# Kernel optimization log

Measured on AMD Instinct MI355X. Metric: run time of the kernel, lower is better.

The kernel has to match this reference:

```python
import jax, jax.numpy as jnp
import numpy as np

B, L, E, H = 2, 2048, 1024, 16
D = E // H  # 64


def setup_inputs() -> dict:
    key = jax.random.key(0)
    ks = jax.random.split(key, 9)
    return {
        "query": jax.random.normal(ks[0], (B, L, E), dtype=jnp.float32),
        "value": jax.random.normal(ks[1], (B, L, E), dtype=jnp.float32),
        "key": jax.random.normal(ks[2], (B, L, E), dtype=jnp.float32),
        "mask": jax.random.randint(ks[3], (B, 1, L, L), 0, 2, dtype=jnp.int32),
        "Wq": jax.random.normal(ks[4], (D, D), dtype=jnp.float32) * 0.05,
        "Wk": jax.random.normal(ks[5], (D, D), dtype=jnp.float32) * 0.05,
        "Wv": jax.random.normal(ks[6], (D, D), dtype=jnp.float32) * 0.05,
        "Wfc": jax.random.normal(ks[7], (E, E), dtype=jnp.float32) * 0.02,
        "bfc": jax.random.normal(ks[8], (E,), dtype=jnp.float32) * 0.02,
    }


def reference(query, value, key, mask, Wq, Wk, Wv, Wfc, bfc):
    b, q_len, _ = query.shape
    k_len = key.shape[1]
    v_len = value.shape[1]
    # split heads: [b, l, H, D]
    q = query.reshape(b, q_len, H, D)
    k = key.reshape(b, k_len, H, D)
    v = value.reshape(b, v_len, H, D)
    # per-head linear projections (shared weights across heads, no bias)
    q = jnp.einsum('bqhd,ed->bqhe', q, Wq)
    k = jnp.einsum('bkhd,ed->bkhe', k, Wk)
    v = jnp.einsum('bvhd,ed->bvhe', v, Wv)
    # attention scores [b, H, q, k]
    attn = jnp.einsum('bqhd,bkhd->bhqk', q, k)
    # NOTE: original masks BEFORE scaling, and scales by sqrt(embedding_size)
    attn = jnp.where(mask == 0, jnp.float32(-1e20), attn)
    attn = attn / jnp.float32(E ** 0.5)
    attn = jax.nn.softmax(attn, axis=3)
    out = jnp.einsum('bhqk,bkhd->bqhd', attn, v).reshape(b, q_len, E)
    out = out @ Wfc.T + bfc
    return out
```

## Files before the change

### kernel.cpp

```cpp
#include <hip/hip_runtime.h>
#include <hip/hip_bf16.h>


#define B_ 2
#define L_ 2048
#define E_ 1024
#define H_ 16
#define D_ 64

typedef __attribute__((ext_vector_type(8))) short s8v;
typedef __attribute__((ext_vector_type(4))) float f4v;
typedef __attribute__((ext_vector_type(2))) float f2v;

__device__ __forceinline__ f4v mfma16(s8v a, s8v b, f4v c) {
    return __builtin_amdgcn_mfma_f32_16x16x32_bf16(a, b, c, 0, 0, 0);
}

__device__ __forceinline__ float fast_exp2(float x) {
    return __builtin_amdgcn_exp2f(x);
}

__device__ __forceinline__ ushort bf16bits(float f) {
    __hip_bfloat16 h = __float2bfloat16(f);
    return *(ushort*)&h;
}

__device__ __forceinline__ void glds16(const __hip_bfloat16* g, ushort* l) {
    __builtin_amdgcn_global_load_lds(
        (const __attribute__((address_space(1))) void*)g,
        (__attribute__((address_space(3))) void*)l,
        16, 0, 0);
}

__device__ __forceinline__ s8v ld8_dual(const void* p, size_t idx, bool isf32) {
    if (isf32) {
        const float* pf = (const float*)p + idx;
        f4v f0 = *(const f4v*)pf;
        f4v f1 = *(const f4v*)(pf + 4);
        s8v r;
        r[0] = (short)bf16bits(f0[0]); r[1] = (short)bf16bits(f0[1]);
        r[2] = (short)bf16bits(f0[2]); r[3] = (short)bf16bits(f0[3]);
        r[4] = (short)bf16bits(f1[0]); r[5] = (short)bf16bits(f1[1]);
        r[6] = (short)bf16bits(f1[2]); r[7] = (short)bf16bits(f1[3]);
        return r;
    }
    return *(const s8v*)((const __hip_bfloat16*)p + idx);
}

__device__ __forceinline__ s8v ld8_ws(const __hip_bfloat16* p) {
    return *(const s8v*)p;
}

__device__ __forceinline__ s8v u4_to_s8(uint a, uint b, uint c, uint d) {
    union { uint u[4]; s8v v; } x;
    x.u[0] = a; x.u[1] = b; x.u[2] = c; x.u[3] = d;
    return x.v;
}

__device__ __forceinline__ void cvt_piece(
    size_t i4, const void* Wfc, const void* bfc,
    __hip_bfloat16* wfc_bf, __hip_bfloat16* bfc_bf, bool isf32)
{
    const size_t base = i4 * 4;
    const size_t n1 = (size_t)E_ * E_;
    if (base >= n1 + E_) return;
    const void* src = (base < n1) ? Wfc : bfc;
    const size_t off = (base < n1) ? base : base - n1;
    __hip_bfloat16* dst = (base < n1) ? (wfc_bf + off) : (bfc_bf + off);
    if (isf32) {
        f4v v = *(const f4v*)((const float*)src + off);
        #pragma unroll
        for (int j = 0; j < 4; ++j) dst[j] = __float2bfloat16(v[j]);
    } else {
        *(ushort4*)dst = *(const ushort4*)((const ushort*)src + off);
    }
}

__global__ void detect_kernel(const ushort* __restrict__ q, int* __restrict__ flag) {
    __shared__ int cnt;
    if (threadIdx.x == 0) cnt = 0;
    __syncthreads();
    int bad = 0;
    #pragma unroll
    for (int i = 0; i < 16; ++i) {
        ushort u = q[threadIdx.x * 16 + i];
        int e = (u >> 7) & 0xFF;
        if (e >= 0x8E) ++bad;
    }
    atomicAdd(&cnt, bad);
    __syncthreads();
    if (threadIdx.x == 0) *flag = (cnt > 100) ? 1 : 0;
}

__global__ __launch_bounds__(256) void proj_all_kernel(
    const void* __restrict__ q_in, const void* __restrict__ k_in,
    const void* __restrict__ v_in,
    const void* __restrict__ Wq, const void* __restrict__ Wk,
    const void* __restrict__ Wv,
    const void* __restrict__ Wfc, const void* __restrict__ bfc,
    const int* __restrict__ mask, unsigned long long* __restrict__ mbits,
    __hip_bfloat16* __restrict__ qp, __hip_bfloat16* __restrict__ kp,
    __hip_bfloat16* __restrict__ vpT,
    __hip_bfloat16* __restrict__ wfc_bf, __hip_bfloat16* __restrict__ bfc_bf,
    const int* __restrict__ flag)
{
    __shared__ __align__(16) ushort tile[64][72];
    const bool isf32 = (*flag != 0);
    const int wave = threadIdx.x >> 6;
    const int lane = threadIdx.x & 63;
    const int quad = lane >> 4;
    const int l16  = lane & 15;

    if (blockIdx.y == 3) {
        const int lane_ = threadIdx.x & 63;
        const size_t wbase = (size_t)blockIdx.x * 128 + wave * 32;
        #pragma unroll 4
        for (int i = 0; i < 32; ++i) {
            const size_t widx = wbase + i;
            const int v = mask[widx * 64 + lane_];
            const unsigned long long bal = __ballot(v != 0);
            if (lane_ == 0) mbits[widx] = bal;
        }
        return;
    }
    if (blockIdx.y == 4) {
        cvt_piece((size_t)blockIdx.x * 256 + threadIdx.x, Wfc, bfc, wfc_bf, bfc_bf, isf32);
        if (blockIdx.x == 0)
            cvt_piece((size_t)(E_ * (size_t)E_ / 4) + threadIdx.x, Wfc, bfc, wfc_bf, bfc_bf, isf32);
        return;
    }
    if (blockIdx.y < 2) {
        const void* X = blockIdx.y == 0 ? q_in : k_in;
        const void* W = blockIdx.y == 0 ? Wq : Wk;
        __hip_bfloat16* dst = blockIdx.y == 0 ? qp : kp;
        const float oscale = (blockIdx.y == 0) ? 0.045084439755930314f : 1.0f;
        const int m0 = (blockIdx.x * 4 + wave) * 16;

        const size_t abase = (size_t)(m0 + l16) * D_;
        s8v a0 = ld8_dual(X, abase + quad * 8, isf32);
        s8v a1 = ld8_dual(X, abase + 32 + quad * 8, isf32);

        f4v acc[4];
        #pragma unroll
        for (int nt = 0; nt < 4; ++nt) {
            const size_t bbase = (size_t)(nt * 16 + l16) * D_;
            s8v b0 = ld8_dual(W, bbase + quad * 8, isf32);
            s8v b1 = ld8_dual(W, bbase + 32 + quad * 8, isf32);
            f4v c = {0.f, 0.f, 0.f, 0.f};
            c = mfma16(a0, b0, c);
            c = mfma16(a1, b1, c);
            acc[nt] = c;
        }
        #pragma unroll
        for (int r = 0; r < 4; ++r) {
            const int m = m0 + quad * 4 + r;
            const int h = m & 15;
            const int bl = m >> 4;
            const int b = bl >> 11;
            const int l = bl & (L_ - 1);
            #pragma unroll
            for (int nt = 0; nt < 4; ++nt) {
                const int e = nt * 16 + l16;
                dst[(((size_t)(b * H_ + h)) * L_ + l) * D_ + e] =
                    __float2bfloat16(acc[nt][r] * oscale);
            }
        }
    } else {
        const int l0 = (blockIdx.x & 31) * 64;
        const int bh = blockIdx.x >> 5;
        const int b = bh >> 4, h = bh & 15;
        const int lw = l0 + wave * 16;

        const size_t xbase = ((size_t)(b * L_ + lw + l16)) * E_ + h * D_;
        s8v a0 = ld8_dual(v_in, xbase + quad * 8, isf32);
        s8v a1 = ld8_dual(v_in, xbase + 32 + quad * 8, isf32);

        #pragma unroll
        for (int nt = 0; nt < 4; ++nt) {
            const int e = nt * 16 + l16;
            s8v b0 = ld8_dual(Wv, (size_t)e * D_ + quad * 8, isf32);
            s8v b1 = ld8_dual(Wv, (size_t)e * D_ + 32 + quad * 8, isf32);
            f4v c = {0.f, 0.f, 0.f, 0.f};
            c = mfma16(a0, b0, c);
            c = mfma16(a1, b1, c);
            #pragma unroll
            for (int r = 0; r < 4; ++r)
                tile[wave * 16 + quad * 4 + r][e] = bf16bits(c[r]);
        }
        __syncthreads();
        const int e  = threadIdx.x >> 2;
        const int lc = (threadIdx.x & 3) * 16;
        s8v s0, s1;
        #pragma unroll
        for (int i = 0; i < 8; ++i) {
            s0[i] = (short)tile[lc + i][e];
            s1[i] = (short)tile[lc + 8 + i][e];
        }
        __hip_bfloat16* drow = vpT + ((size_t)bh * D_ + e) * L_ + l0 + lc;
        *(s8v*)drow = s0;
        *(s8v*)(drow + 8) = s1;
    }
}

__global__ __launch_bounds__(256) void cvt_wfc_kernel(
    const void* __restrict__ Wfc, const void* __restrict__ bfc,
    __hip_bfloat16* __restrict__ wfc_bf, __hip_bfloat16* __restrict__ bfc_bf,
    const int* __restrict__ flag)
{
    cvt_piece((size_t)blockIdx.x * 256 + threadIdx.x, Wfc, bfc, wfc_bf, bfc_bf, *flag != 0);
}

__global__ __launch_bounds__(256, 4) void attn_kernel(
    const __hip_bfloat16* __restrict__ qp,
    const __hip_bfloat16* __restrict__ kp,
    const __hip_bfloat16* __restrict__ vpT,
    const unsigned long long* __restrict__ mbits,
    __hip_bfloat16* __restrict__ attn_out)
{
    __shared__ __align__(16) ushort kbuf[2][64 * 64];
    __shared__ __align__(16) ushort vbuf[2][64 * 64];

    const int wave = threadIdx.x >> 6;
    const int lane = threadIdx.x & 63;
    const int quad = lane >> 4;
    const int l16  = lane & 15;
    const int sw   = l16 & 7;
    const int bh = blockIdx.y;
    const int b = bh >> 4, h = bh & 15;
    const int q0 = blockIdx.x * 64 + wave * 16;

    const __hip_bfloat16* kbh = kp + (size_t)bh * L_ * D_;
    const __hip_bfloat16* vbh = vpT + (size_t)bh * D_ * L_;
    const unsigned long long* mrow = mbits + ((size_t)b * L_ + q0 + l16) * 32;

    const int lrow = lane >> 3;
    const int lchk = (lane & 7) ^ lrow;
    const int r0 = wave * 16;
    const __hip_bfloat16* kg0 = kbh + (size_t)(r0 + lrow) * D_ + lchk * 8;
    const __hip_bfloat16* kg1 = kbh + (size_t)(r0 + 8 + lrow) * D_ + lchk * 8;
    const __hip_bfloat16* vg0 = vbh + (size_t)(r0 + lrow) * L_ + lchk * 8;
    const __hip_bfloat16* vg1 = vbh + (size_t)(r0 + 8 + lrow) * L_ + lchk * 8;

    const __hip_bfloat16* qbase = qp + ((size_t)bh * L_ + q0) * D_;
    s8v qa0 = ld8_ws(qbase + (size_t)l16 * D_ + quad * 8);
    s8v qa1 = ld8_ws(qbase + (size_t)l16 * D_ + 32 + quad * 8);

    f2v rs2 = {0.f, 0.f};
    f4v o[4];
    #pragma unroll
    for (int nt = 0; nt < 4; ++nt) o[nt] = (f4v){0.f, 0.f, 0.f, 0.f};

    glds16(kg0, &kbuf[0][r0 * 64]);
    glds16(kg1, &kbuf[0][r0 * 64 + 512]);
    glds16(vg0, &vbuf[0][r0 * 64]);
    glds16(vg1, &vbuf[0][r0 * 64 + 512]);
    __syncthreads();

    const int shq = quad * 4;
    int cur = 0;
    for (int it = 0; it < 32; ++it) {
        const int k0 = it * 64;
        const unsigned long long wq = mrow[it];
        const uint wlo_sh = ((uint)wq) >> shq;
        const uint whi_sh = ((uint)(wq >> 32)) >> shq;
        if (it < 31) {
            glds16(kg0 + (size_t)(k0 + 64) * D_, &kbuf[cur ^ 1][r0 * 64]);
            glds16(kg1 + (size_t)(k0 + 64) * D_, &kbuf[cur ^ 1][r0 * 64 + 512]);
            glds16(vg0 + (k0 + 64), &vbuf[cur ^ 1][r0 * 64]);
            glds16(vg1 + (k0 + 64), &vbuf[cur ^ 1][r0 * 64 + 512]);
        }
        f4v s[4];
        #pragma unroll
        for (int nt = 0; nt < 4; ++nt) {
            const ushort* kr = &kbuf[cur][(nt * 16 + l16) * 64];
            s8v kb0 = *(const s8v*)(kr + ((quad ^ sw) << 3));
            s8v kb1 = *(const s8v*)(kr + (((quad + 4) ^ sw) << 3));
            f4v c = {0.f, 0.f, 0.f, 0.f};
            c = mfma16(kb0, qa0, c);
            c = mfma16(kb1, qa1, c);
            s[nt] = c;
        }
        uint dw[4][2];
        #pragma unroll
        for (int nt = 0; nt < 4; ++nt) {
            const uint hs = (nt & 2) ? whi_sh : wlo_sh;
            float pr[4];
            #pragma unroll
            for (int r = 0; r < 4; ++r) {
                const float p = fast_exp2(s[nt][r]);
                const int m = __builtin_amdgcn_sbfe((int)hs, ((nt & 1) << 4) + r, 1);
                pr[r] = __uint_as_float(__float_as_uint(p) & (uint)m);
            }
            rs2 += (f2v){pr[0], pr[1]};
            rs2 += (f2v){pr[2], pr[3]};
            asm("v_cvt_pk_bf16_f32 %0, %1, %2"
                : "=v"(dw[nt][0]) : "v"(pr[0]), "v"(pr[1]));
            asm("v_cvt_pk_bf16_f32 %0, %1, %2"
                : "=v"(dw[nt][1]) : "v"(pr[2]), "v"(pr[3]));
        }
        uint w00 = dw[0][0], w10 = dw[1][0];
        uint w01 = dw[0][1], w11 = dw[1][1];
        uint w20 = dw[2][0], w30 = dw[3][0];
        uint w21 = dw[2][1], w31 = dw[3][1];
        asm("v_permlane32_swap_b32 %0, %1" : "+v"(w00), "+v"(w10));
        asm("v_permlane16_swap_b32 %0, %1" : "+v"(w00), "+v"(w10));
        asm("v_permlane32_swap_b32 %0, %1" : "+v"(w01), "+v"(w11));
        asm("v_permlane16_swap_b32 %0, %1" : "+v"(w01), "+v"(w11));
        asm("v_permlane32_swap_b32 %0, %1" : "+v"(w20), "+v"(w30));
        asm("v_permlane16_swap_b32 %0, %1" : "+v"(w20), "+v"(w30));
        asm("v_permlane32_swap_b32 %0, %1" : "+v"(w21), "+v"(w31));
        asm("v_permlane16_swap_b32 %0, %1" : "+v"(w21), "+v"(w31));
        s8v pa0 = u4_to_s8(w00, w01, w10, w11);
        s8v pa1 = u4_to_s8(w20, w21, w30, w31);
        #pragma unroll
        for (int nt = 0; nt < 4; ++nt) {
            const ushort* vr = &vbuf[cur][(nt * 16 + l16) * 64];
            s8v vb0 = *(const s8v*)(vr + ((quad ^ sw) << 3));
            s8v vb1 = *(const s8v*)(vr + (((quad + 4) ^ sw) << 3));
            o[nt] = mfma16(pa0, vb0, o[nt]);
            o[nt] = mfma16(pa1, vb1, o[nt]);
        }
        __syncthreads();
        cur ^= 1;
    }
    float v = rs2[0] + rs2[1];
    v += __shfl_xor(v, 16, 64);
    v += __shfl_xor(v, 32, 64);
    #pragma unroll
    for (int r = 0; r < 4; ++r) {
        const int qrow = quad * 4 + r;
        const float li = __shfl(v, qrow, 64);
        const float inv = 1.0f / fmaxf(li, 1e-30f);
        const int row = q0 + qrow;
        #pragma unroll
        for (int nt = 0; nt < 4; ++nt) {
            const int d = nt * 16 + l16;
            attn_out[((size_t)(b * L_ + row)) * E_ + h * D_ + d] =
                __float2bfloat16(o[nt][r] * inv);
        }
    }
}

__global__ __launch_bounds__(256, 4) void fc_kernel(
    const __hip_bfloat16* __restrict__ x,
    const __hip_bfloat16* __restrict__ wfc_bf,
    const __hip_bfloat16* __restrict__ bfc_bf,
    void* __restrict__ out, const int* __restrict__ flag)
{
    __shared__ __align__(16) ushort abuf[2][64 * 64];
    __shared__ __align__(16) ushort bbuf[2][64 * 64];
    const bool isf32 = (*flag != 0);
    const int wave = threadIdx.x >> 6;
    const int lane = threadIdx.x & 63;
    const int quad = lane >> 4;
    const int l16  = lane & 15;
    const int sw   = l16 & 7;
    const int m0 = blockIdx.x * 64;
    const int n0 = blockIdx.y * 64;

    const int lrow = lane >> 3;
    const int lchk = (lane & 7) ^ lrow;
    const int r0 = wave * 16;
    const __hip_bfloat16* ag0 = x + (size_t)(m0 + r0 + lrow) * E_ + lchk * 8;
    const __hip_bfloat16* ag1 = x + (size_t)(m0 + r0 + 8 + lrow) * E_ + lchk * 8;
    const __hip_bfloat16* bg0 = wfc_bf + (size_t)(n0 + r0 + lrow) * E_ + lchk * 8;
    const __hip_bfloat16* bg1 = wfc_bf + (size_t)(n0 + r0 + 8 + lrow) * E_ + lchk * 8;

    f4v acc[4];
    #pragma unroll
    for (int nt = 0; nt < 4; ++nt) acc[nt] = (f4v){0.f, 0.f, 0.f, 0.f};

    glds16(ag0, &abuf[0][r0 * 64]);
    glds16(ag1, &abuf[0][r0 * 64 + 512]);
    glds16(bg0, &bbuf[0][r0 * 64]);
    glds16(bg1, &bbuf[0][r0 * 64 + 512]);
    __syncthreads();

    int cur = 0;
    for (int it = 0; it < 16; ++it) {
        const int k0 = it * 64;
        if (it < 15) {
            glds16(ag0 + k0 + 64, &abuf[cur ^ 1][r0 * 64]);
            glds16(ag1 + k0 + 64, &abuf[cur ^ 1][r0 * 64 + 512]);
            glds16(bg0 + k0 + 64, &bbuf[cur ^ 1][r0 * 64]);
            glds16(bg1 + k0 + 64, &bbuf[cur ^ 1][r0 * 64 + 512]);
        }
        const ushort* ar = &abuf[cur][(r0 + l16) * 64];
        s8v a0 = *(const s8v*)(ar + ((quad ^ sw) << 3));
        s8v a1 = *(const s8v*)(ar + (((quad + 4) ^ sw) << 3));
        #pragma unroll
        for (int nt = 0; nt < 4; ++nt) {
            const ushort* br = &bbuf[cur][(nt * 16 + l16) * 64];
            s8v b0 = *(const s8v*)(br + ((quad ^ sw) << 3));
            s8v b1 = *(const s8v*)(br + (((quad + 4) ^ sw) << 3));
            acc[nt] = mfma16(a0, b0, acc[nt]);
            acc[nt] = mfma16(a1, b1, acc[nt]);
        }
        __syncthreads();
        cur ^= 1;
    }
    #pragma unroll
    for (int r = 0; r < 4; ++r) {
        const int m = m0 + r0 + quad * 4 + r;
        #pragma unroll
        for (int nt = 0; nt < 4; ++nt) {
            const int n = n0 + nt * 16 + l16;
            const float val = acc[nt][r] + __bfloat162float(bfc_bf[n]);
            if (isf32) ((float*)out)[(size_t)m * E_ + n] = val;
            else       ((__hip_bfloat16*)out)[(size_t)m * E_ + n] = __float2bfloat16(val);
        }
    }
}

extern "C" void kernel_launch(void* const* d_in, const int* in_sizes, int n_in,
                              void* d_out, int out_size, void* d_ws, size_t ws_size,
                              hipStream_t stream) {
    const void* query = d_in[0];
    const void* value = d_in[1];
    const void* key   = d_in[2];
    const int*  mask  = (const int*)d_in[3];
    const void* Wq  = d_in[4];
    const void* Wk  = d_in[5];
    const void* Wv  = d_in[6];
    const void* Wfc = d_in[7];
    const void* bfc = d_in[8];

    char* ws = (char*)d_ws;
    int* flag                     = (int*)ws;
    unsigned long long* mbits     = (unsigned long long*)(ws + (64u << 10));
    __hip_bfloat16* qp            = (__hip_bfloat16*)(ws + (2u  << 20));
    __hip_bfloat16* kp            = (__hip_bfloat16*)(ws + (10u << 20));
    __hip_bfloat16* vpT           = (__hip_bfloat16*)(ws + (18u << 20));
    __hip_bfloat16* attn_out      = (__hip_bfloat16*)(ws + (26u << 20));

    const bool big_ws = ws_size >= (37ull << 20);
    __hip_bfloat16* wfc_bf = big_ws ? (__hip_bfloat16*)(ws + (34ull << 20)) : qp;
    __hip_bfloat16* bfc_bf = wfc_bf + (size_t)E_ * E_;

    detect_kernel<<<1, 256, 0, stream>>>((const ushort*)query, flag);
    proj_all_kernel<<<dim3(1024, big_ws ? 5 : 4), 256, 0, stream>>>(
        query, key, value, Wq, Wk, Wv, Wfc, bfc, mask, mbits,
        qp, kp, vpT, wfc_bf, bfc_bf, flag);
    attn_kernel<<<dim3(32, 32), 256, 0, stream>>>(qp, kp, vpT, mbits, attn_out);
    if (!big_ws)
        cvt_wfc_kernel<<<1025, 256, 0, stream>>>(Wfc, bfc, wfc_bf, bfc_bf, flag);
    fc_kernel<<<dim3(64, 16), 256, 0, stream>>>(attn_out, wfc_bf, bfc_bf, d_out, flag);
}
```

Measured before the change: 242.8 us.

## Software-pipeline QK^T one tile ahead of softmax and PV in attention loop

Computes the score MFMAs for the next key tile while the current tile's exponentials, masking and PV MFMAs run, with a prologue that computes the first tile before the loop. K loads are issued two tiles ahead and V loads one tile ahead, using separate buffer indices. The aim is to let the matrix cores overlap with the VALU exp/pack/permlane work and hide the QK dependency latency. It costs extra registers for the carried score tile and makes the buffer indexing more involved.

```diff
diff --git a/kernel.cpp b/kernel.cpp
--- a/kernel.cpp
+++ b/kernel.cpp
@@ -255,30 +255,47 @@
     glds16(vg0, &vbuf[0][r0 * 64]);
     glds16(vg1, &vbuf[0][r0 * 64 + 512]);
     __syncthreads();
+    glds16(kg0 + (size_t)64 * D_, &kbuf[1][r0 * 64]);
+    glds16(kg1 + (size_t)64 * D_, &kbuf[1][r0 * 64 + 512]);
+    f4v S[4];
+    #pragma unroll
+    for (int nt = 0; nt < 4; ++nt) {
+        const ushort* kr = &kbuf[0][(nt * 16 + l16) * 64];
+        s8v kb0 = *(const s8v*)(kr + ((quad ^ sw) << 3));
+        s8v kb1 = *(const s8v*)(kr + (((quad + 4) ^ sw) << 3));
+        f4v c = {0.f, 0.f, 0.f, 0.f};
+        c = mfma16(kb0, qa0, c);
+        c = mfma16(kb1, qa1, c);
+        S[nt] = c;
+    }
+    __syncthreads();
 
     const int shq = quad * 4;
-    int cur = 0;
+    int ck = 1, cv = 0;
     for (int it = 0; it < 32; ++it) {
-        const int k0 = it * 64;
         const unsigned long long wq = mrow[it];
         const uint wlo_sh = ((uint)wq) >> shq;
         const uint whi_sh = ((uint)(wq >> 32)) >> shq;
         if (it < 31) {
-            glds16(kg0 + (size_t)(k0 + 64) * D_, &kbuf[cur ^ 1][r0 * 64]);
-            glds16(kg1 + (size_t)(k0 + 64) * D_, &kbuf[cur ^ 1][r0 * 64 + 512]);
-            glds16(vg0 + (k0 + 64), &vbuf[cur ^ 1][r0 * 64]);
-            glds16(vg1 + (k0 + 64), &vbuf[cur ^ 1][r0 * 64 + 512]);
-        }
-        f4v s[4];
-        #pragma unroll
-        for (int nt = 0; nt < 4; ++nt) {
-            const ushort* kr = &kbuf[cur][(nt * 16 + l16) * 64];
-            s8v kb0 = *(const s8v*)(kr + ((quad ^ sw) << 3));
-            s8v kb1 = *(const s8v*)(kr + (((quad + 4) ^ sw) << 3));
-            f4v c = {0.f, 0.f, 0.f, 0.f};
-            c = mfma16(kb0, qa0, c);
-            c = mfma16(kb1, qa1, c);
-            s[nt] = c;
+            glds16(vg0 + (it + 1) * 64, &vbuf[cv ^ 1][r0 * 64]);
+            glds16(vg1 + (it + 1) * 64, &vbuf[cv ^ 1][r0 * 64 + 512]);
+            if (it < 30) {
+                glds16(kg0 + (size_t)(it + 2) * 64 * D_, &kbuf[ck ^ 1][r0 * 64]);
+                glds16(kg1 + (size_t)(it + 2) * 64 * D_, &kbuf[ck ^ 1][r0 * 64 + 512]);
+            }
+        }
+        f4v Sn[4];
+        if (it < 31) {
+            #pragma unroll
+            for (int nt = 0; nt < 4; ++nt) {
+                const ushort* kr = &kbuf[ck][(nt * 16 + l16) * 64];
+                s8v kb0 = *(const s8v*)(kr + ((quad ^ sw) << 3));
+                s8v kb1 = *(const s8v*)(kr + (((quad + 4) ^ sw) << 3));
+                f4v c = {0.f, 0.f, 0.f, 0.f};
+                c = mfma16(kb0, qa0, c);
+                c = mfma16(kb1, qa1, c);
+                Sn[nt] = c;
+            }
         }
         uint dw[4][2];
         #pragma unroll
@@ -287,7 +304,7 @@
             float pr[4];
             #pragma unroll
             for (int r = 0; r < 4; ++r) {
-                const float p = fast_exp2(s[nt][r]);
+                const float p = fast_exp2(S[nt][r]);
                 const int m = __builtin_amdgcn_sbfe((int)hs, ((nt & 1) << 4) + r, 1);
                 pr[r] = __uint_as_float(__float_as_uint(p) & (uint)m);
             }
@@ -314,14 +331,16 @@
         s8v pa1 = u4_to_s8(w20, w21, w30, w31);
         #pragma unroll
         for (int nt = 0; nt < 4; ++nt) {
-            const ushort* vr = &vbuf[cur][(nt * 16 + l16) * 64];
+            const ushort* vr = &vbuf[cv][(nt * 16 + l16) * 64];
             s8v vb0 = *(const s8v*)(vr + ((quad ^ sw) << 3));
             s8v vb1 = *(const s8v*)(vr + (((quad + 4) ^ sw) << 3));
             o[nt] = mfma16(pa0, vb0, o[nt]);
             o[nt] = mfma16(pa1, vb1, o[nt]);
         }
         __syncthreads();
-        cur ^= 1;
+        #pragma unroll
+        for (int nt = 0; nt < 4; ++nt) S[nt] = Sn[nt];
+        ck ^= 1; cv ^= 1;
     }
     float v = rs2[0] + rs2[1];
     v += __shfl_xor(v, 16, 64);
```

Result: no change. 238.3 us (-1.9%).
